# Kernel optimization log

Measured on AMD Instinct MI355X. Metric: run time of the kernel, lower is better.

Reference implementation:

```python
import jax, jax.numpy as jnp
import numpy as np

WIN = 21            # window_pixel_wh
SIGMA = 2.0
B, H, W, C = 16, 1008, 1008, 1
HS, WS = H // WIN, W // WIN      # 48, 48 window grid
T = HS * WS                      # num_tracks = 2304
P = WIN * WIN                    # 441 pixels per window


def _build_constants():
    # Window-center positions mapped to logical coords in [-1, 1]
    xs, ys = np.meshgrid(np.arange(WS, dtype=np.float32) * WIN,
                         np.arange(HS, dtype=np.float32) * WIN)
    px = xs + WIN // 2
    py = ys + WIN // 2
    win_pos = np.stack([2.0 * px / W - 1.0, 2.0 * py / H - 1.0], axis=-1)
    win_pos = win_pos.reshape(1, T, 1, 2).astype(np.float32)
    # Gaussian window weights: exp(-r^2 / (2 sigma^2)) over pixel radius.
    c = WIN // 2
    yy, xx = np.mgrid[0:WIN, 0:WIN]
    r2 = ((xx - c) ** 2 + (yy - c) ** 2).astype(np.float32)
    weights = np.exp(-r2 / (2.0 * SIGMA ** 2)).reshape(1, 1, P, 1).astype(np.float32)
    center_rel = np.array([W / WIN, H / WIN], dtype=np.float32).reshape(1, 1, 1, 2)
    sx = np.array([[-3, 0, 3], [-10, 0, 10], [-3, 0, 3]], np.float32).reshape(3, 3, 1, 1)
    sy = np.array([[-3, -10, -3], [0, 0, 0], [3, 10, 3]], np.float32).reshape(3, 3, 1, 1)
    return (jnp.asarray(win_pos), jnp.asarray(weights), jnp.asarray(center_rel),
            jnp.asarray(sx), jnp.asarray(sy))

WIN_POS, WEIGHTS, CENTER_REL, SCHARR_X, SCHARR_Y = _build_constants()


def _split_windows(img):
    o = img[:, :HS * WIN, :WS * WIN]
    o = o.reshape(-1, HS, WIN, WS, WIN, C)
    return o.transpose(0, 1, 3, 2, 4, 5).reshape(-1, T, WIN, WIN, C)


def setup_inputs() -> dict:
    key = jax.random.key(0)
    imgs = jax.random.uniform(key, (B, 2, H, W, C), dtype=jnp.float32)
    return {"imgs": imgs}


def reference(imgs):
    ff = imgs[:, 0]   # first frame  [B,H,W,C]
    sf = imgs[:, 1]   # second frame
    dn = ('NHWC', 'HWIO', 'NHWC')
    ff_dx = jax.lax.conv_general_dilated(ff, SCHARR_X, (1, 1), 'SAME', dimension_numbers=dn)
    ff_dy = jax.lax.conv_general_dilated(ff, SCHARR_Y, (1, 1), 'SAME', dimension_numbers=dn)

    ffw = _split_windows(ff)
    sfw = _split_windows(sf)
    Ix = _split_windows(ff_dx).reshape(-1, T, P, 1)
    Iy = _split_windows(ff_dy).reshape(-1, T, P, 1)

    A = jnp.concatenate([Ix, Iy], axis=3)          # [B,T,P,2]
    ATA = jnp.einsum('btpi,btpj->btij', A, A * WEIGHTS)  # [B,T,2,2]
    a = ATA[..., 0, 0]; b = ATA[..., 0, 1]
    c = ATA[..., 1, 0]; d = ATA[..., 1, 1]
    det = a * d - b * c
    inv_det = jnp.where(det != 0.0, 1.0 / jnp.where(det != 0.0, det, 1.0), 0.0)  # divide_no_nan
    # tf: stack([stack([d,-b],-1), stack([-c,a],-1)], axis=3)
    ATA_inv = inv_det[..., None, None] * jnp.stack(
        [jnp.stack([d, -b], axis=-1), jnp.stack([-c, a], axis=-1)], axis=3)

    rhs = -(sfw - ffw).reshape(-1, T, P, 1) * WEIGHTS   # [B,T,P,1]
    ATb = jnp.einsum('btpi,btpk->btik', A, rhs)          # [B,T,2,1]
    VxVy = ATA_inv @ ATb                                 # [B,T,2,1]

    vels = VxVy.transpose(0, 1, 3, 2)                    # [B,T,1,2]
    vels = vels / CENTER_REL + WIN_POS
    wp = jnp.broadcast_to(WIN_POS, vels.shape)
    return jnp.concatenate([wp, vels], axis=2)           # [B,T,2,2]
```

## Files before the change

kernel.cpp:

```cpp
#include <hip/hip_runtime.h>


constexpr int HH   = 1008;
constexpr int WW   = 1008;
constexpr int WINN = 21;
constexpr int HSN  = 48;
constexpr int WSN  = 48;
constexpr int TN   = HSN * WSN;

__device__ __constant__ const float kWY[WINN] = {
    3.7266532e-6f, 4.0065297e-5f, 3.3546262e-4f, 2.1874911e-3f,
    1.1108997e-2f, 4.3936934e-2f, 1.3533528e-1f, 3.2465247e-1f,
    6.0653066e-1f, 8.8249690e-1f, 1.0f,          8.8249690e-1f,
    6.0653066e-1f, 3.2465247e-1f, 1.3533528e-1f, 4.3936934e-2f,
    1.1108997e-2f, 2.1874911e-3f, 3.3546262e-4f, 4.0065297e-5f,
    3.7266532e-6f };

struct Row { float4 v; float l, r; };

__device__ __forceinline__ Row zero_row() {
    Row z; z.v = make_float4(0.f, 0.f, 0.f, 0.f); z.l = 0.f; z.r = 0.f;
    return z;
}

__device__ __forceinline__ Row load_row(const float* __restrict__ rp,
                                        int c0, int ln, bool act) {
    Row r;
    float4 v = make_float4(0.f, 0.f, 0.f, 0.f);
    if (act) v = *reinterpret_cast<const float4*>(rp + c0);
    r.v = v;
    r.l = __shfl_up(v.w, 1);
    r.r = __shfl_down(v.x, 1);
    if (ln == 0)  r.l = (c0 > 0)       ? rp[c0 - 1] : 0.0f;
    if (ln == 62) r.r = (c0 + 4 < WW)  ? rp[c0 + 4] : 0.0f;
    return r;
}

__global__ __launch_bounds__(256)
void SparseOptFlowLK_kernel(const float* __restrict__ imgs,
                            float* __restrict__ out) {
    const int bi = blockIdx.x;
    const int b  = bi / HSN;
    const int hy = bi % HSN;

    const float* __restrict__ ff = imgs + (size_t)b * (2ull * HH * WW);
    const float* __restrict__ sf = ff + (size_t)HH * WW;

    __shared__ float4 colsum4[5][WW / 4];
    __shared__ float  red[WSN][5];

    const int  lx  = threadIdx.x;
    const int  wv  = lx >> 6;
    const int  ln  = lx & 63;
    const bool act = (ln < 63);
    const int  c0  = wv * 252 + 4 * ln;

    const int g0 = hy * WINN;

    float wx[4];
    {
        int m = c0 % WINN;
        #pragma unroll
        for (int c = 0; c < 4; ++c) {
            int mc = m + c; if (mc >= WINN) mc -= WINN;
            const float dx = (float)(mc - 10);
            wx[c] = __expf(-dx * dx * 0.125f);
        }
    }

    Row rt = (g0 > 0) ? load_row(ff + (size_t)(g0 - 1) * WW, c0, ln, act)
                      : zero_row();
    Row rm = load_row(ff + (size_t)g0 * WW, c0, ln, act);

    float sA[4] = {0,0,0,0}, sB[4] = {0,0,0,0}, sD[4] = {0,0,0,0};
    float sX[4] = {0,0,0,0}, sY[4] = {0,0,0,0};

    #pragma unroll
    for (int y = 0; y < WINN; ++y) {
        const int gp = g0 + y + 1;
        Row rb = (gp < HH) ? load_row(ff + (size_t)gp * WW, c0, ln, act)
                           : zero_row();
        float4 sfv = make_float4(0.f, 0.f, 0.f, 0.f);
        if (act) sfv = *reinterpret_cast<const float4*>(
                           sf + (size_t)(g0 + y) * WW + c0);

        const float wy = kWY[y];

        const float T[6] = { rt.l, rt.v.x, rt.v.y, rt.v.z, rt.v.w, rt.r };
        const float M[6] = { rm.l, rm.v.x, rm.v.y, rm.v.z, rm.v.w, rm.r };
        const float Bo[6] = { rb.l, rb.v.x, rb.v.y, rb.v.z, rb.v.w, rb.r };
        const float SF[4] = { sfv.x, sfv.y, sfv.z, sfv.w };

        #pragma unroll
        for (int c = 0; c < 4; ++c) {
            const float Ix = 3.0f * (T[c+2] - T[c]) + 10.0f * (M[c+2] - M[c])
                           + 3.0f * (Bo[c+2] - Bo[c]);
            const float Iy = 3.0f * (Bo[c] - T[c]) + 10.0f * (Bo[c+1] - T[c+1])
                           + 3.0f * (Bo[c+2] - T[c+2]);
            const float df = M[c+1] - SF[c];
            const float w  = wx[c] * wy;
            const float wIx = w * Ix, wIy = w * Iy;
            sA[c] += wIx * Ix;
            sB[c] += wIx * Iy;
            sD[c] += wIy * Iy;
            sX[c] += wIx * df;
            sY[c] += wIy * df;
        }
        rt = rm; rm = rb;
    }

    if (act) {
        const int ci = wv * 63 + ln;
        colsum4[0][ci] = make_float4(sA[0], sA[1], sA[2], sA[3]);
        colsum4[1][ci] = make_float4(sB[0], sB[1], sB[2], sB[3]);
        colsum4[2][ci] = make_float4(sD[0], sD[1], sD[2], sD[3]);
        colsum4[3][ci] = make_float4(sX[0], sX[1], sX[2], sX[3]);
        colsum4[4][ci] = make_float4(sY[0], sY[1], sY[2], sY[3]);
    }
    __syncthreads();

    if (lx < WSN * 5) {
        const int w = lx / 5;
        const int s = lx % 5;
        const float* cs = reinterpret_cast<const float*>(colsum4)
                        + s * WW + w * WINN;
        float sum = 0.0f;
        #pragma unroll
        for (int j = 0; j < WINN; ++j) sum += cs[j];
        red[w][s] = sum;
    }
    __syncthreads();

    if (lx < WSN) {
        const float A  = red[lx][0];
        const float Bv = red[lx][1];
        const float D  = red[lx][2];
        const float Bx = red[lx][3];
        const float By = red[lx][4];

        const float det = A * D - Bv * Bv;
        const float inv = (det != 0.0f) ? (1.0f / det) : 0.0f;
        const float vx  = inv * ( D * Bx - Bv * By);
        const float vy  = inv * (-Bv * Bx + A  * By);

        const float wpx = 2.0f * (float)(lx * WINN + WINN / 2) / (float)WW - 1.0f;
        const float wpy = 2.0f * (float)(hy * WINN + WINN / 2) / (float)HH - 1.0f;

        float4 o;
        o.x = wpx;
        o.y = wpy;
        o.z = vx / 48.0f + wpx;
        o.w = vy / 48.0f + wpy;
        reinterpret_cast<float4*>(out)[(size_t)b * TN + hy * WSN + lx] = o;
    }
}

extern "C" void kernel_launch(void* const* d_in, const int* in_sizes, int n_in,
                              void* d_out, int out_size, void* d_ws, size_t ws_size,
                              hipStream_t stream) {
    const float* imgs = (const float*)d_in[0];
    float* out = (float*)d_out;

    const int B = in_sizes[0] / (2 * HH * WW);
    const dim3 grid(B * HSN);
    SparseOptFlowLK_kernel<<<grid, 256, 0, stream>>>(imgs, out);
}
```

Baseline: 203.6 us.

## Split window-row blocks by column segment and row chunks across waves

Each block now covers one quarter of the image width (12 windows), and its four waves each handle a chunk of the 21 rows instead of a quarter of the columns. All row loads are issued upfront into registers, and the per-wave partial sums are combined through shared memory. The aim is to raise the block count and expose more independent memory loads per thread to hide latency. In exchange, halo rows are loaded redundantly at chunk boundaries, register pressure rises, and the final wave does only half as much work as the others.

```diff
diff --git a/kernel.cpp b/kernel.cpp
--- a/kernel.cpp
+++ b/kernel.cpp
@@ -7,8 +7,10 @@
 constexpr int HSN  = 48;
 constexpr int WSN  = 48;
 constexpr int TN   = HSN * WSN;
+constexpr int SEGS = 4;
+constexpr int WPB  = WSN / SEGS;
 
-__device__ __constant__ const float kWY[WINN] = {
+__device__ __constant__ float kWY[WINN] = {
     3.7266532e-6f, 4.0065297e-5f, 3.3546262e-4f, 2.1874911e-3f,
     1.1108997e-2f, 4.3936934e-2f, 1.3533528e-1f, 3.2465247e-1f,
     6.0653066e-1f, 8.8249690e-1f, 1.0f,          8.8249690e-1f,
@@ -16,50 +18,66 @@
     1.1108997e-2f, 2.1874911e-3f, 3.3546262e-4f, 4.0065297e-5f,
     3.7266532e-6f };
 
-struct Row { float4 v; float l, r; };
-
-__device__ __forceinline__ Row zero_row() {
-    Row z; z.v = make_float4(0.f, 0.f, 0.f, 0.f); z.l = 0.f; z.r = 0.f;
-    return z;
-}
-
-__device__ __forceinline__ Row load_row(const float* __restrict__ rp,
-                                        int c0, int ln, bool act) {
-    Row r;
-    float4 v = make_float4(0.f, 0.f, 0.f, 0.f);
-    if (act) v = *reinterpret_cast<const float4*>(rp + c0);
-    r.v = v;
-    r.l = __shfl_up(v.w, 1);
-    r.r = __shfl_down(v.x, 1);
-    if (ln == 0)  r.l = (c0 > 0)       ? rp[c0 - 1] : 0.0f;
-    if (ln == 62) r.r = (c0 + 4 < WW)  ? rp[c0 + 4] : 0.0f;
-    return r;
-}
-
-__global__ __launch_bounds__(256)
+__global__ __launch_bounds__(256, 4)
 void SparseOptFlowLK_kernel(const float* __restrict__ imgs,
                             float* __restrict__ out) {
-    const int bi = blockIdx.x;
-    const int b  = bi / HSN;
-    const int hy = bi % HSN;
+    const int bi  = blockIdx.x;
+    const int b   = bi / (HSN * SEGS);
+    const int rem = bi % (HSN * SEGS);
+    const int hy  = rem / SEGS;
+    const int seg = rem % SEGS;
 
     const float* __restrict__ ff = imgs + (size_t)b * (2ull * HH * WW);
     const float* __restrict__ sf = ff + (size_t)HH * WW;
 
-    __shared__ float4 colsum4[5][WW / 4];
-    __shared__ float  red[WSN][5];
+    __shared__ float partial[4][5][256];
+    __shared__ float red[WPB][5];
 
     const int  lx  = threadIdx.x;
     const int  wv  = lx >> 6;
     const int  ln  = lx & 63;
     const bool act = (ln < 63);
-    const int  c0  = wv * 252 + 4 * ln;
+    const int  c0  = seg * 252 + 4 * ln;
+    const int  r0  = 6 * wv;
+    const int  nr  = (wv == 3) ? 3 : 6;
+    const int  g0  = hy * WINN;
 
-    const int g0 = hy * WINN;
+    float4 ffv[8];
+    #pragma unroll
+    for (int i = 0; i < 8; ++i) {
+        ffv[i] = make_float4(0.f, 0.f, 0.f, 0.f);
+        const int gr = g0 + r0 - 1 + i;
+        if (act && i <= nr + 1 && gr >= 0 && gr < HH)
+            ffv[i] = *reinterpret_cast<const float4*>(ff + (size_t)gr * WW + c0);
+    }
+    float4 sfv[6];
+    #pragma unroll
+    for (int i = 0; i < 6; ++i) {
+        sfv[i] = make_float4(0.f, 0.f, 0.f, 0.f);
+        if (act && i < nr)
+            sfv[i] = *reinterpret_cast<const float4*>(
+                         sf + (size_t)(g0 + r0 + i) * WW + c0);
+    }
+
+    float ffl[8], ffr[8];
+    #pragma unroll
+    for (int i = 0; i < 8; ++i) {
+        ffl[i] = __shfl_up(ffv[i].w, 1);
+        ffr[i] = __shfl_down(ffv[i].x, 1);
+    }
+    #pragma unroll
+    for (int i = 0; i < 8; ++i) {
+        const int  gr = g0 + r0 - 1 + i;
+        const bool rv = (i <= nr + 1 && gr >= 0 && gr < HH);
+        if (ln == 0)
+            ffl[i] = (rv && c0 > 0)      ? ff[(size_t)gr * WW + c0 - 1] : 0.f;
+        if (ln == 62)
+            ffr[i] = (rv && c0 + 4 < WW) ? ff[(size_t)gr * WW + c0 + 4] : 0.f;
+    }
 
     float wx[4];
     {
-        int m = c0 % WINN;
+        const int m = c0 % WINN;
         #pragma unroll
         for (int c = 0; c < 4; ++c) {
             int mc = m + c; if (mc >= WINN) mc -= WINN;
@@ -68,70 +86,63 @@
         }
     }
 
-    Row rt = (g0 > 0) ? load_row(ff + (size_t)(g0 - 1) * WW, c0, ln, act)
-                      : zero_row();
-    Row rm = load_row(ff + (size_t)g0 * WW, c0, ln, act);
-
     float sA[4] = {0,0,0,0}, sB[4] = {0,0,0,0}, sD[4] = {0,0,0,0};
     float sX[4] = {0,0,0,0}, sY[4] = {0,0,0,0};
 
     #pragma unroll
-    for (int y = 0; y < WINN; ++y) {
-        const int gp = g0 + y + 1;
-        Row rb = (gp < HH) ? load_row(ff + (size_t)gp * WW, c0, ln, act)
-                           : zero_row();
-        float4 sfv = make_float4(0.f, 0.f, 0.f, 0.f);
-        if (act) sfv = *reinterpret_cast<const float4*>(
-                           sf + (size_t)(g0 + y) * WW + c0);
+    for (int yl = 0; yl < 6; ++yl) {
+        if (yl < nr) {
+            const float wy = kWY[r0 + yl];
+            const float T[6]  = { ffl[yl],   ffv[yl].x,   ffv[yl].y,
+                                  ffv[yl].z, ffv[yl].w,   ffr[yl] };
+            const float M[6]  = { ffl[yl+1], ffv[yl+1].x, ffv[yl+1].y,
+                                  ffv[yl+1].z, ffv[yl+1].w, ffr[yl+1] };
+            const float Bo[6] = { ffl[yl+2], ffv[yl+2].x, ffv[yl+2].y,
+                                  ffv[yl+2].z, ffv[yl+2].w, ffr[yl+2] };
+            const float SF[4] = { sfv[yl].x, sfv[yl].y, sfv[yl].z, sfv[yl].w };
 
-        const float wy = kWY[y];
-
-        const float T[6] = { rt.l, rt.v.x, rt.v.y, rt.v.z, rt.v.w, rt.r };
-        const float M[6] = { rm.l, rm.v.x, rm.v.y, rm.v.z, rm.v.w, rm.r };
-        const float Bo[6] = { rb.l, rb.v.x, rb.v.y, rb.v.z, rb.v.w, rb.r };
-        const float SF[4] = { sfv.x, sfv.y, sfv.z, sfv.w };
-
-        #pragma unroll
-        for (int c = 0; c < 4; ++c) {
-            const float Ix = 3.0f * (T[c+2] - T[c]) + 10.0f * (M[c+2] - M[c])
-                           + 3.0f * (Bo[c+2] - Bo[c]);
-            const float Iy = 3.0f * (Bo[c] - T[c]) + 10.0f * (Bo[c+1] - T[c+1])
-                           + 3.0f * (Bo[c+2] - T[c+2]);
-            const float df = M[c+1] - SF[c];
-            const float w  = wx[c] * wy;
-            const float wIx = w * Ix, wIy = w * Iy;
-            sA[c] += wIx * Ix;
-            sB[c] += wIx * Iy;
-            sD[c] += wIy * Iy;
-            sX[c] += wIx * df;
-            sY[c] += wIy * df;
+            #pragma unroll
+            for (int c = 0; c < 4; ++c) {
+                const float Ix = 3.0f * (T[c+2] - T[c]) + 10.0f * (M[c+2] - M[c])
+                               + 3.0f * (Bo[c+2] - Bo[c]);
+                const float Iy = 3.0f * (Bo[c] - T[c]) + 10.0f * (Bo[c+1] - T[c+1])
+                               + 3.0f * (Bo[c+2] - T[c+2]);
+                const float df = M[c+1] - SF[c];
+                const float w  = wx[c] * wy;
+                const float wIx = w * Ix, wIy = w * Iy;
+                sA[c] += wIx * Ix;
+                sB[c] += wIx * Iy;
+                sD[c] += wIy * Iy;
+                sX[c] += wIx * df;
+                sY[c] += wIy * df;
+            }
         }
-        rt = rm; rm = rb;
     }
 
     if (act) {
-        const int ci = wv * 63 + ln;
-        colsum4[0][ci] = make_float4(sA[0], sA[1], sA[2], sA[3]);
-        colsum4[1][ci] = make_float4(sB[0], sB[1], sB[2], sB[3]);
-        colsum4[2][ci] = make_float4(sD[0], sD[1], sD[2], sD[3]);
-        colsum4[3][ci] = make_float4(sX[0], sX[1], sX[2], sX[3]);
-        colsum4[4][ci] = make_float4(sY[0], sY[1], sY[2], sY[3]);
+        *reinterpret_cast<float4*>(&partial[wv][0][4*ln]) = make_float4(sA[0],sA[1],sA[2],sA[3]);
+        *reinterpret_cast<float4*>(&partial[wv][1][4*ln]) = make_float4(sB[0],sB[1],sB[2],sB[3]);
+        *reinterpret_cast<float4*>(&partial[wv][2][4*ln]) = make_float4(sD[0],sD[1],sD[2],sD[3]);
+        *reinterpret_cast<float4*>(&partial[wv][3][4*ln]) = make_float4(sX[0],sX[1],sX[2],sX[3]);
+        *reinterpret_cast<float4*>(&partial[wv][4][4*ln]) = make_float4(sY[0],sY[1],sY[2],sY[3]);
     }
     __syncthreads();
 
-    if (lx < WSN * 5) {
-        const int w = lx / 5;
+    if (lx < WPB * 5) {
+        const int k = lx / 5;
         const int s = lx % 5;
-        const float* cs = reinterpret_cast<const float*>(colsum4)
-                        + s * WW + w * WINN;
         float sum = 0.0f;
         #pragma unroll
-        for (int j = 0; j < WINN; ++j) sum += cs[j];
-        red[w][s] = sum;
+        for (int w4 = 0; w4 < 4; ++w4) {
+            #pragma unroll
+            for (int j = 0; j < WINN; ++j)
+                sum += partial[w4][s][k * WINN + j];
+        }
+        red[k][s] = sum;
     }
     __syncthreads();
 
-    if (lx < WSN) {
+    if (lx < WPB) {
         const float A  = red[lx][0];
         const float Bv = red[lx][1];
         const float D  = red[lx][2];
@@ -143,15 +154,16 @@
         const float vx  = inv * ( D * Bx - Bv * By);
         const float vy  = inv * (-Bv * Bx + A  * By);
 
-        const float wpx = 2.0f * (float)(lx * WINN + WINN / 2) / (float)WW - 1.0f;
-        const float wpy = 2.0f * (float)(hy * WINN + WINN / 2) / (float)HH - 1.0f;
+        const int wxg = seg * WPB + lx;
+        const float wpx = 2.0f * (float)(wxg * WINN + WINN / 2) / (float)WW - 1.0f;
+        const float wpy = 2.0f * (float)(hy  * WINN + WINN / 2) / (float)HH - 1.0f;
 
         float4 o;
         o.x = wpx;
         o.y = wpy;
         o.z = vx / 48.0f + wpx;
         o.w = vy / 48.0f + wpy;
-        reinterpret_cast<float4*>(out)[(size_t)b * TN + hy * WSN + lx] = o;
+        reinterpret_cast<float4*>(out)[(size_t)b * TN + hy * WSN + wxg] = o;
     }
 }
 
@@ -162,6 +174,6 @@
     float* out = (float*)d_out;
 
     const int B = in_sizes[0] / (2 * HH * WW);
-    const dim3 grid(B * HSN);
+    const dim3 grid(B * HSN * SEGS);
     SparseOptFlowLK_kernel<<<grid, 256, 0, stream>>>(imgs, out);
 }
```

Measured after the change: 189.0 us. 1.08x faster.
